# Kernel tuning notes

Hardware: AMD Instinct MI355X
Metric: run time of the kernel (lower is better)

The kernel has to match this reference:

```python
import jax, jax.numpy as jnp
import numpy as np

T = 4096          # timesteps
INPUT_DIM = 360   # n_static + 9*n_dynamic + 8
H2 = 512          # hidden2 (startMap out)
E = 128           # embed_size
H = 1024          # hidden_dim
OUT = 512         # output_dim


def setup_inputs() -> dict:
    key = jax.random.key(0)
    ks = jax.random.split(key, 9)

    def p(k, shape, fan_in):
        return (jax.random.normal(k, shape, dtype=jnp.float32) / np.float32(np.sqrt(fan_in)))

    return {
        "inputVecs": jax.random.normal(ks[0], (T, INPUT_DIM), dtype=jnp.float32),
        # startMap: Linear(input_dim -> hidden2)
        "Ws": p(ks[1], (H2, INPUT_DIM), INPUT_DIM),
        "bs": jnp.zeros((H2,), jnp.float32),
        # LSTM layer 1: input = hidden2 + embed_size
        "W_ih1": p(ks[2], (4 * H, H2 + E), H2 + E),
        "W_hh1": p(ks[3], (4 * H, H), H),
        "b_ih1": jnp.zeros((4 * H,), jnp.float32),
        "b_hh1": jnp.zeros((4 * H,), jnp.float32),
        # LSTM layer 2: input = hidden_dim
        "W_ih2": p(ks[4], (4 * H, H), H),
        "W_hh2": p(ks[5], (4 * H, H), H),
        "b_ih2": jnp.zeros((4 * H,), jnp.float32),
        "b_hh2": jnp.zeros((4 * H,), jnp.float32),
        # linear: Linear(hidden_dim -> output_dim)
        "Wl": p(ks[6], (OUT, H), H),
        "bl": jnp.zeros((OUT,), jnp.float32),
        # map: Linear(output_dim -> embed_size)
        "Wm": p(ks[7], (E, OUT), OUT),
        "bm": jnp.zeros((E,), jnp.float32),
    }


def _lstm_cell(x, h, c, W_ih, W_hh, b_ih, b_hh):
    # torch LSTM gate order: i, f, g, o
    gates = W_ih @ x + b_ih + W_hh @ h + b_hh
    i, f, g, o = jnp.split(gates, 4)
    c_new = jax.nn.sigmoid(f) * c + jax.nn.sigmoid(i) * jnp.tanh(g)
    h_new = jax.nn.sigmoid(o) * jnp.tanh(c_new)
    return h_new, c_new


def reference(inputVecs, Ws, bs, W_ih1, W_hh1, b_ih1, b_hh1,
              W_ih2, W_hh2, b_ih2, b_hh2, Wl, bl, Wm, bm):
    H_ = W_hh1.shape[1]
    E_ = Wm.shape[0]

    def step(carry, x_t):
        h1, c1, h2, c2, embed = carry
        feat = Ws @ x_t + bs                       # [H2]
        inp = jnp.concatenate([feat, embed])       # [H2+E]
        h1, c1 = _lstm_cell(inp, h1, c1, W_ih1, W_hh1, b_ih1, b_hh1)
        h2, c2 = _lstm_cell(h1, h2, c2, W_ih2, W_hh2, b_ih2, b_hh2)
        y = Wl @ h2 + bl                           # [OUT]
        new_embed = Wm @ jax.nn.log_softmax(y) + bm  # feedback embed for next step
        return (h1, c1, h2, c2, new_embed), y

    z = jnp.zeros((H_,), inputVecs.dtype)
    init = (z, z, z, z, jnp.zeros((E_,), inputVecs.dtype))
    _, ys = jax.lax.scan(step, init, inputVecs)    # ys: [T, OUT]
    return jax.nn.log_softmax(ys, axis=1)
```

## Files before the change

kernel.cpp:

```cpp
#include <hip/hip_runtime.h>
#include <math.h>


#define T_STEPS 4096
#define NWG 256

typedef unsigned u32x4 __attribute__((ext_vector_type(4)));

#define WS_RH1   0
#define WS_RH2   16384
#define WS_RY    32768
#define WS_ZERO_BYTES 40960
#define WS_FEAT  40960

#define OFF_WA 2560
#define OFF_WB 18944
#define OFF_WY 31232
#define SMEM_FLOATS 33280
#define SMEM_BYTES  (SMEM_FLOATS*4)

#define PIN4(v) asm volatile("" : "+v"((v).x), "+v"((v).y), "+v"((v).z), "+v"((v).w))
#define PIN1(v) asm volatile("" : "+v"(v))
#define FMA4(acc,s,v4) {(acc).x += (s)*(v4).x; (acc).y += (s)*(v4).y; (acc).z += (s)*(v4).z; (acc).w += (s)*(v4).w;}
#define DOT4(a,b) ((a).x*(b).x + (a).y*(b).y + (a).z*(b).z + (a).w*(b).w)

__device__ __forceinline__ u32x4 ld16(const u32x4* p){
  u32x4 r;
  asm volatile("global_load_dwordx4 %0, %1, off sc0 sc1\n\ts_waitcnt vmcnt(0)"
               : "=v"(r) : "v"(p) : "memory");
  return r;
}
__device__ __forceinline__ void ld16x4(const u32x4* p, u32x4& r0, u32x4& r1,
                                       u32x4& r2, u32x4& r3){
  asm volatile("global_load_dwordx4 %0, %4, off sc0 sc1\n\t"
               "global_load_dwordx4 %1, %4, off offset:16 sc0 sc1\n\t"
               "global_load_dwordx4 %2, %4, off offset:32 sc0 sc1\n\t"
               "global_load_dwordx4 %3, %4, off offset:48 sc0 sc1\n\t"
               "s_waitcnt vmcnt(0)"
               : "=&v"(r0), "=&v"(r1), "=&v"(r2), "=&v"(r3)
               : "v"(p) : "memory");
}
__device__ __forceinline__ void st16(u32x4* p, u32x4 v){
  asm volatile("global_store_dwordx4 %0, %1, off sc0 sc1"
               :: "v"(p), "v"(v) : "memory");
}
__device__ __forceinline__ float sigm(float x){ return 1.0f/(1.0f+expf(-x)); }

__global__ __launch_bounds__(512) void feat_kernel(
    const float* __restrict__ x, const float* __restrict__ Ws,
    const float* __restrict__ bs, float* __restrict__ feat)
{
  __shared__ float s_x[16][360];
  __shared__ float s_w[512][20];
  const int bid = blockIdx.x, tid = threadIdx.x;
  const int t0 = bid * 16;
  for (int tt = 0; tt < 16; tt++)
    if (tid < 360) s_x[tt][tid] = x[(t0+tt)*360 + tid];
  float acc[16];
  #pragma unroll
  for (int i = 0; i < 16; i++) acc[i] = 0.f;
  for (int d0 = 0; d0 < 360; d0 += 16){
    const int dn = (360 - d0 < 16) ? (360 - d0) : 16;
    __syncthreads();
    if (dn == 16){
      #pragma unroll
      for (int c4 = 0; c4 < 4; c4++)
        *(float4*)&s_w[tid][c4*4] = *(const float4*)&Ws[tid*360 + d0 + c4*4];
    } else {
      for (int c = 0; c < dn; c++) s_w[tid][c] = Ws[tid*360 + d0 + c];
    }
    __syncthreads();
    for (int c = 0; c < dn; c++){
      float wv = s_w[tid][c];
      #pragma unroll
      for (int tt = 0; tt < 16; tt++) acc[tt] += wv * s_x[tt][d0 + c];
    }
  }
  for (int tt = 0; tt < 16; tt++)
    feat[(t0+tt)*512 + tid] = acc[tt] + bs[tid];
}

__global__ __launch_bounds__(64) void ls_kernel(float* __restrict__ out)
{
  const int t = blockIdx.x, l = threadIdx.x;
  float v[8];
  #pragma unroll
  for (int i = 0; i < 8; i++) v[i] = out[t*512 + l*8 + i];
  float m0 = v[0];
  #pragma unroll
  for (int i = 1; i < 8; i++) m0 = fmaxf(m0, v[i]);
  #pragma unroll
  for (int mk = 32; mk; mk >>= 1) m0 = fmaxf(m0, __shfl_xor(m0, mk));
  float s = 0.f;
  #pragma unroll
  for (int i = 0; i < 8; i++) s += expf(v[i] - m0);
  #pragma unroll
  for (int mk = 32; mk; mk >>= 1) s += __shfl_xor(s, mk);
  float lse = m0 + logf(s);
  #pragma unroll
  for (int i = 0; i < 8; i++) out[t*512 + l*8 + i] = v[i] - lse;
}

__global__ __launch_bounds__(512, 1) void lstm_persist(
    const float* __restrict__ Wih1, const float* __restrict__ Whh1,
    const float* __restrict__ Wih2, const float* __restrict__ Whh2,
    const float* __restrict__ Wl,   const float* __restrict__ Wm,
    const float* __restrict__ bih1, const float* __restrict__ bhh1,
    const float* __restrict__ bih2, const float* __restrict__ bhh2,
    const float* __restrict__ blp,  const float* __restrict__ bmp,
    char* __restrict__ wsb, float* __restrict__ out)
{
  extern __shared__ float smem[];
  float* s_in = smem;
  float* wa   = smem + OFF_WA;
  float* wb   = smem + OFF_WB;
  float* wy   = smem + OFF_WY;
  __shared__ float s_part[16];
  __shared__ float s_sums[32];

  u32x4* rh1 = (u32x4*)(wsb + WS_RH1);
  u32x4* rh2 = (u32x4*)(wsb + WS_RH2);
  u32x4* ry  = (u32x4*)(wsb + WS_RY);
  const float* featp = (const float*)(wsb + WS_FEAT);

  const int wid = blockIdx.x, tid = threadIdx.x;
  const int w = tid >> 6, l = tid & 63;
  const int o0 = 2*w, o1 = 2*w + 1;
  const int rA0 = (o0 >> 2)*1024 + wid*4 + (o0 & 3);
  const int rA1 = (o1 >> 2)*1024 + wid*4 + (o1 & 3);

  for (int idx = tid; idx < 2048; idx += 512){
    int o = idx >> 7, e = idx & 127;
    int r = (o >> 2)*1024 + wid*4 + (o & 3);
    s_in[idx] = Wih1[r*640 + 512 + e];
  }
  __syncthreads();

  {
    float4 a00 = {0,0,0,0}, a01 = a00, a10 = a00, a11 = a00;
    for (int e = 0; e < 128; e++){
      float w0e = s_in[o0*128 + e], w1e = s_in[o1*128 + e];
      float4 m0 = *(const float4*)&Wm[e*512 + l*4];
      float4 m1 = *(const float4*)&Wm[e*512 + l*4 + 256];
      FMA4(a00, w0e, m0); FMA4(a01, w0e, m1);
      FMA4(a10, w1e, m0); FMA4(a11, w1e, m1);
    }
    *(float4*)&wb[o0*512 + l*4]       = a00;
    *(float4*)&wb[o0*512 + l*4 + 256] = a01;
    *(float4*)&wb[o1*512 + l*4]       = a10;
    *(float4*)&wb[o1*512 + l*4 + 256] = a11;
  }
  __syncthreads();

  {
    float4 c00={0,0,0,0}, c01=c00, c02=c00, c03=c00;
    float4 c10=c00, c11=c00, c12=c00, c13=c00;
    float rs0=0.f, rs1=0.f, wl0=0.f, wl1=0.f;
    for (int m = 0; m < 512; m++){
      float t0 = wb[o0*512 + m], t1 = wb[o1*512 + m];
      float blm = blp[m];
      rs0 += t0; wl0 += t0*blm; rs1 += t1; wl1 += t1*blm;
      float4 q0 = *(const float4*)&Wl[m*1024 + l*4];
      float4 q1 = *(const float4*)&Wl[m*1024 + l*4 + 256];
      float4 q2 = *(const float4*)&Wl[m*1024 + l*4 + 512];
      float4 q3 = *(const float4*)&Wl[m*1024 + l*4 + 768];
      FMA4(c00,t0,q0); FMA4(c01,t0,q1); FMA4(c02,t0,q2); FMA4(c03,t0,q3);
      FMA4(c10,t1,q0); FMA4(c11,t1,q1); FMA4(c12,t1,q2); FMA4(c13,t1,q3);
    }
    *(float4*)&wa[o0*1024 + l*4      ] = c00;
    *(float4*)&wa[o0*1024 + l*4 + 256] = c01;
    *(float4*)&wa[o0*1024 + l*4 + 512] = c02;
    *(float4*)&wa[o0*1024 + l*4 + 768] = c03;
    *(float4*)&wa[o1*1024 + l*4      ] = c10;
    *(float4*)&wa[o1*1024 + l*4 + 256] = c11;
    *(float4*)&wa[o1*1024 + l*4 + 512] = c12;
    *(float4*)&wa[o1*1024 + l*4 + 768] = c13;
    if (l == 0){
      s_sums[w*4+0] = rs0; s_sums[w*4+1] = rs1;
      s_sums[w*4+2] = wl0; s_sums[w*4+3] = wl1;
    }
  }
  __syncthreads();

  float biasAreg=0.f, biasBreg=0.f, bE2reg=0.f, rsReg=0.f;
  float bl0=0.f, bl1=0.f, c1=0.f, c2=0.f;
  if (w == 0 && l < 16){
    int r = (l >> 2)*1024 + wid*4 + (l & 3);
    biasAreg = bih1[r] + bhh1[r];
    biasBreg = bih2[r] + bhh2[r];
    rsReg = s_sums[(l>>1)*4 + (l&1)];
    float acc = s_sums[(l>>1)*4 + 2 + (l&1)];
    for (int e = 0; e < 128; e++) acc += s_in[l*128 + e] * bmp[e];
    bE2reg = acc;
  }
  if (w == 0 && l == 0){ bl0 = blp[wid*2]; bl1 = blp[wid*2 + 1]; }
  __syncthreads();

  for (int idx = tid; idx < 2048; idx += 512) s_in[512 + idx] = 0.f;
  for (int o = 0; o < 16; o++){
    int r = (o >> 2)*1024 + wid*4 + (o & 3);
    for (int c = tid; c < 768; c += 512)
      wb[o*768 + c] = Whh2[r*1024 + 256 + c];
  }
  for (int idx = tid; idx < 2048; idx += 512){
    int row = idx >> 10, c = idx & 1023;
    wy[idx] = Wl[(wid*2 + row)*1024 + c];
  }

  float4 wA0[6], wA1[6], wB0[5], wB1[5];
  #pragma unroll
  for (int j = 0; j < 6; j++){
    int c = 256*j + l*4;
    wA0[j] = (c < 512) ? *(const float4*)&Wih1[rA0*640 + c]
                       : *(const float4*)&Whh1[rA0*1024 + c - 512];
    wA1[j] = (c < 512) ? *(const float4*)&Wih1[rA1*640 + c]
                       : *(const float4*)&Whh1[rA1*1024 + c - 512];
  }
  #pragma unroll
  for (int j = 0; j < 5; j++){
    int c = 256*j + l*4;
    wB0[j] = (c < 1024) ? *(const float4*)&Wih2[rA0*1024 + c]
                        : *(const float4*)&Whh2[rA0*1024 + c - 1024];
    wB1[j] = (c < 1024) ? *(const float4*)&Wih2[rA1*1024 + c]
                        : *(const float4*)&Whh2[rA1*1024 + c - 1024];
  }
  #pragma unroll
  for (int j = 0; j < 6; j++){ PIN4(wA0[j]); PIN4(wA1[j]); }
  #pragma unroll
  for (int j = 0; j < 5; j++){ PIN4(wB0[j]); PIN4(wB1[j]); }
  PIN1(biasAreg); PIN1(biasBreg); PIN1(bE2reg); PIN1(rsReg);
  PIN1(bl0); PIN1(bl1);
  __syncthreads();

  for (int t = 0; t < T_STEPS; t++){
    const int pprev = (t + 1) & 1;
    const int pcur  = t & 1;

    if (tid < 256)
      *(float2*)&s_in[tid*2] = *(const float2*)&featp[(size_t)t*512 + tid*2];
    __syncthreads();

    float acc0 = 0.f, acc1 = 0.f;
    #pragma unroll
    for (int j = 0; j < 6; j++){
      float4 xv = *(float4*)&s_in[256*j + l*4];
      acc0 += DOT4(wA0[j], xv); acc1 += DOT4(wA1[j], xv);
    }

    if (t > 0){
      const u32x4* p2 = rh2 + pprev*512 + tid;
      u32x4 b;
      for(;;){
        b = ld16(p2);
        if (b.z >= (unsigned)t) break;
        __builtin_amdgcn_s_sleep(1);
      }
      *(float2*)&s_in[1536 + 2*tid] =
          make_float2(__uint_as_float(b.x), __uint_as_float(b.y));
    }
    __syncthreads();

    if (t > 0 && w == 0){
      float y0 = 0.f, y1 = 0.f;
      #pragma unroll
      for (int i = 0; i < 4; i++){
        float4 xv = *(float4*)&s_in[1536 + 256*i + l*4];
        float4 w0 = *(float4*)&wy[256*i + l*4];
        float4 w1 = *(float4*)&wy[1024 + 256*i + l*4];
        y0 += DOT4(w0, xv); y1 += DOT4(w1, xv);
      }
      #pragma unroll
      for (int mk = 32; mk; mk >>= 1){
        y0 += __shfl_xor(y0, mk); y1 += __shfl_xor(y1, mk);
      }
      if (l == 0){
        y0 += bl0; y1 += bl1;
        *(float2*)&out[(size_t)(t-1)*512 + wid*2] = make_float2(y0, y1);
        u32x4 rec;
        rec.x = __float_as_uint(y0); rec.y = __float_as_uint(y1);
        rec.z = (unsigned)t; rec.w = 0u;
        st16(ry + pcur*256 + wid, rec);
      }
    }
    #pragma unroll
    for (int k = 0; k < 4; k++){
      float4 xv = *(float4*)&s_in[1536 + 256*k + l*4];
      float4 u0 = *(float4*)&wa[o0*1024 + 256*k + l*4];
      float4 u1 = *(float4*)&wa[o1*1024 + 256*k + l*4];
      acc0 += DOT4(u0, xv); acc1 += DOT4(u1, xv);
    }
    #pragma unroll
    for (int mk = 32; mk; mk >>= 1){
      acc0 += __shfl_xor(acc0, mk); acc1 += __shfl_xor(acc1, mk);
    }
    if (l == 0){ s_part[o0] = acc0; s_part[o1] = acc1; }

    float pB0, pB1;
    {
      float4 xv = *(float4*)&s_in[1536 + l*4];
      pB0 = DOT4(wB0[4], xv); pB1 = DOT4(wB1[4], xv);
      #pragma unroll
      for (int k = 0; k < 3; k++){
        float4 x2 = *(float4*)&s_in[1536 + 256 + 256*k + l*4];
        float4 u0 = *(float4*)&wb[o0*768 + 256*k + l*4];
        float4 u1 = *(float4*)&wb[o1*768 + 256*k + l*4];
        pB0 += DOT4(u0, x2); pB1 += DOT4(u1, x2);
      }
    }
    __syncthreads();

    if (w == 0){
      float lse = 0.f;
      if (t > 0){
        const u32x4* pyr = ry + pcur*256 + 4*l;
        u32x4 r0, r1, r2, r3;
        for(;;){
          ld16x4(pyr, r0, r1, r2, r3);
          if (r0.z >= (unsigned)t && r1.z >= (unsigned)t &&
              r2.z >= (unsigned)t && r3.z >= (unsigned)t) break;
          __builtin_amdgcn_s_sleep(1);
        }
        float v0 = __uint_as_float(r0.x), v1 = __uint_as_float(r0.y);
        float v2 = __uint_as_float(r1.x), v3 = __uint_as_float(r1.y);
        float v4 = __uint_as_float(r2.x), v5 = __uint_as_float(r2.y);
        float v6 = __uint_as_float(r3.x), v7 = __uint_as_float(r3.y);
        float m0 = fmaxf(fmaxf(fmaxf(v0,v1), fmaxf(v2,v3)),
                         fmaxf(fmaxf(v4,v5), fmaxf(v6,v7)));
        #pragma unroll
        for (int mk = 32; mk; mk >>= 1) m0 = fmaxf(m0, __shfl_xor(m0, mk));
        float s = expf(v0-m0)+expf(v1-m0)+expf(v2-m0)+expf(v3-m0)
                + expf(v4-m0)+expf(v5-m0)+expf(v6-m0)+expf(v7-m0);
        #pragma unroll
        for (int mk = 32; mk; mk >>= 1) s += __shfl_xor(s, mk);
        lse = m0 + logf(s);
      }
      float hn = 0.f;
      if (l < 16){
        float sum = s_part[l] + biasAreg;
        if (t > 0) sum += bE2reg - rsReg*lse;
        float gi = __shfl(sum, (l & 3));
        float gf = __shfl(sum, 4 + (l & 3));
        float gg = __shfl(sum, 8 + (l & 3));
        float go = __shfl(sum, 12 + (l & 3));
        if (l < 4){
          float cn = sigm(gf)*c1 + sigm(gi)*tanhf(gg);
          c1 = cn;
          hn = sigm(go)*tanhf(cn);
        }
      }
      float g0 = __shfl(hn, 2*(l & 1));
      float g1 = __shfl(hn, 2*(l & 1) + 1);
      if (l < 2){
        u32x4 rec;
        rec.x = __float_as_uint(g0); rec.y = __float_as_uint(g1);
        rec.z = (unsigned)(t + 1); rec.w = 0u;
        st16(rh1 + pcur*512 + wid*2 + l, rec);
      }
    }

    {
      const u32x4* p1 = rh1 + pcur*512 + tid;
      u32x4 a;
      for(;;){
        a = ld16(p1);
        if (a.z >= (unsigned)(t + 1)) break;
        __builtin_amdgcn_s_sleep(1);
      }
      *(float2*)&s_in[512 + 2*tid] =
          make_float2(__uint_as_float(a.x), __uint_as_float(a.y));
    }
    __syncthreads();

    float b0 = pB0, b1 = pB1;
    #pragma unroll
    for (int j = 0; j < 4; j++){
      float4 xv = *(float4*)&s_in[512 + 256*j + l*4];
      b0 += DOT4(wB0[j], xv); b1 += DOT4(wB1[j], xv);
    }
    #pragma unroll
    for (int mk = 32; mk; mk >>= 1){
      b0 += __shfl_xor(b0, mk); b1 += __shfl_xor(b1, mk);
    }
    if (l == 0){ s_part[o0] = b0; s_part[o1] = b1; }
    __syncthreads();

    if (w == 0){
      float hn = 0.f;
      if (l < 16){
        float sum = s_part[l] + biasBreg;
        float gi = __shfl(sum, (l & 3));
        float gf = __shfl(sum, 4 + (l & 3));
        float gg = __shfl(sum, 8 + (l & 3));
        float go = __shfl(sum, 12 + (l & 3));
        if (l < 4){
          float cn = sigm(gf)*c2 + sigm(gi)*tanhf(gg);
          c2 = cn;
          hn = sigm(go)*tanhf(cn);
        }
      }
      float g0 = __shfl(hn, 2*(l & 1));
      float g1 = __shfl(hn, 2*(l & 1) + 1);
      if (l < 2){
        u32x4 rec;
        rec.x = __float_as_uint(g0); rec.y = __float_as_uint(g1);
        rec.z = (unsigned)(t + 1); rec.w = 0u;
        st16(rh2 + pcur*512 + wid*2 + l, rec);
      }
    }
  }

  {
    const u32x4* p2 = rh2 + ((T_STEPS - 1) & 1)*512 + tid;
    u32x4 b;
    for(;;){
      b = ld16(p2);
      if (b.z >= (unsigned)T_STEPS) break;
      __builtin_amdgcn_s_sleep(1);
    }
    *(float2*)&s_in[1536 + 2*tid] =
        make_float2(__uint_as_float(b.x), __uint_as_float(b.y));
  }
  __syncthreads();
  if (w == 0){
    float y0 = 0.f, y1 = 0.f;
    #pragma unroll
    for (int i = 0; i < 4; i++){
      float4 xv = *(float4*)&s_in[1536 + 256*i + l*4];
      float4 w0 = *(float4*)&wy[256*i + l*4];
      float4 w1 = *(float4*)&wy[1024 + 256*i + l*4];
      y0 += DOT4(w0, xv); y1 += DOT4(w1, xv);
    }
    #pragma unroll
    for (int mk = 32; mk; mk >>= 1){
      y0 += __shfl_xor(y0, mk); y1 += __shfl_xor(y1, mk);
    }
    if (l == 0)
      *(float2*)&out[(size_t)(T_STEPS-1)*512 + wid*2] =
          make_float2(y0 + bl0, y1 + bl1);
  }
}

extern "C" void kernel_launch(void* const* d_in, const int* in_sizes, int n_in,
                              void* d_out, int out_size, void* d_ws, size_t ws_size,
                              hipStream_t stream)
{
  const float* x    = (const float*)d_in[0];
  const float* Ws   = (const float*)d_in[1];
  const float* bs   = (const float*)d_in[2];
  const float* Wih1 = (const float*)d_in[3];
  const float* Whh1 = (const float*)d_in[4];
  const float* bih1 = (const float*)d_in[5];
  const float* bhh1 = (const float*)d_in[6];
  const float* Wih2 = (const float*)d_in[7];
  const float* Whh2 = (const float*)d_in[8];
  const float* bih2 = (const float*)d_in[9];
  const float* bhh2 = (const float*)d_in[10];
  const float* Wl   = (const float*)d_in[11];
  const float* bl   = (const float*)d_in[12];
  const float* Wm   = (const float*)d_in[13];
  const float* bm   = (const float*)d_in[14];
  char* wsb  = (char*)d_ws;
  float* out = (float*)d_out;

  hipMemsetAsync(wsb, 0, WS_ZERO_BYTES, stream);

  feat_kernel<<<256, 512, 0, stream>>>(x, Ws, bs, (float*)(wsb + WS_FEAT));
  lstm_persist<<<NWG, 512, SMEM_BYTES, stream>>>(
      Wih1, Whh1, Wih2, Whh2, Wl, Wm,
      bih1, bhh1, bih2, bhh2, bl, bm, wsb, out);
  ls_kernel<<<T_STEPS, 64, 0, stream>>>(out);
}
```

Baseline: 25.11 ms.

## Publish layer-1 pre-activations before lse and apply lse correction redundantly per block

Each workgroup now publishes its raw layer-1 gate pre-activations (without the log-softmax correction) plus its previous cell state to global memory, instead of waiting for the lse reduction before computing and publishing h1. Every workgroup then gathers all gates, applies the per-gate lse correction using precomputed vectors derived from W_ih1 embed columns and Wm column sums, and evaluates the LSTM nonlinearity for all 1024 units redundantly. This takes the lse wait off the critical path of the cross-workgroup handoff, so it overlaps with the exchange. In exchange it doubles the exchanged bytes per step, adds redundant transcendental work in every block, and adds a long setup pass computing the correction vectors.

New measurement: 66.04 ms. 2.63x slower.

```diff
diff --git a/kernel.cpp b/kernel.cpp
--- a/kernel.cpp
+++ b/kernel.cpp
@@ -7,11 +7,11 @@
 
 typedef unsigned u32x4 __attribute__((ext_vector_type(4)));
 
-#define WS_RH1   0
-#define WS_RH2   16384
-#define WS_RY    32768
-#define WS_ZERO_BYTES 40960
-#define WS_FEAT  40960
+#define WS_RG1   0
+#define WS_RH2   65536
+#define WS_RY    81920
+#define WS_ZERO_BYTES 90112
+#define WS_FEAT  90112
 
 #define OFF_WA 2560
 #define OFF_WB 18944
@@ -117,8 +117,11 @@
   float* wy   = smem + OFF_WY;
   __shared__ float s_part[16];
   __shared__ float s_sums[32];
-
-  u32x4* rh1 = (u32x4*)(wsb + WS_RH1);
+  __shared__ float s_cs[128];
+  __shared__ float s_lse[1];
+  __shared__ float s_c1[4];
+
+  u32x4* rg1 = (u32x4*)(wsb + WS_RG1);
   u32x4* rh2 = (u32x4*)(wsb + WS_RH2);
   u32x4* ry  = (u32x4*)(wsb + WS_RY);
   const float* featp = (const float*)(wsb + WS_FEAT);
@@ -133,6 +136,14 @@
     int o = idx >> 7, e = idx & 127;
     int r = (o >> 2)*1024 + wid*4 + (o & 3);
     s_in[idx] = Wih1[r*640 + 512 + e];
+  }
+  if (tid < 128){
+    float s = 0.f;
+    for (int m = 0; m < 512; m += 4){
+      float4 v = *(const float4*)&Wm[tid*512 + m];
+      s += v.x + v.y + v.z + v.w;
+    }
+    s_cs[tid] = s;
   }
   __syncthreads();
 
@@ -155,11 +166,11 @@
   {
     float4 c00={0,0,0,0}, c01=c00, c02=c00, c03=c00;
     float4 c10=c00, c11=c00, c12=c00, c13=c00;
-    float rs0=0.f, rs1=0.f, wl0=0.f, wl1=0.f;
+    float wl0=0.f, wl1=0.f;
     for (int m = 0; m < 512; m++){
       float t0 = wb[o0*512 + m], t1 = wb[o1*512 + m];
       float blm = blp[m];
-      rs0 += t0; wl0 += t0*blm; rs1 += t1; wl1 += t1*blm;
+      wl0 += t0*blm; wl1 += t1*blm;
       float4 q0 = *(const float4*)&Wl[m*1024 + l*4];
       float4 q1 = *(const float4*)&Wl[m*1024 + l*4 + 256];
       float4 q2 = *(const float4*)&Wl[m*1024 + l*4 + 512];
@@ -175,25 +186,43 @@
     *(float4*)&wa[o1*1024 + l*4 + 256] = c11;
     *(float4*)&wa[o1*1024 + l*4 + 512] = c12;
     *(float4*)&wa[o1*1024 + l*4 + 768] = c13;
-    if (l == 0){
-      s_sums[w*4+0] = rs0; s_sums[w*4+1] = rs1;
-      s_sums[w*4+2] = wl0; s_sums[w*4+3] = wl1;
-    }
+    if (l == 0){ s_sums[w*2+0] = wl0; s_sums[w*2+1] = wl1; }
   }
   __syncthreads();
 
-  float biasAreg=0.f, biasBreg=0.f, bE2reg=0.f, rsReg=0.f;
-  float bl0=0.f, bl1=0.f, c1=0.f, c2=0.f;
+  float biasAreg=0.f, biasBreg=0.f, bE2reg=0.f;
+  float bl0=0.f, bl1=0.f, c2=0.f;
   if (w == 0 && l < 16){
     int r = (l >> 2)*1024 + wid*4 + (l & 3);
     biasAreg = bih1[r] + bhh1[r];
     biasBreg = bih2[r] + bhh2[r];
-    rsReg = s_sums[(l>>1)*4 + (l&1)];
-    float acc = s_sums[(l>>1)*4 + 2 + (l&1)];
+    float acc = s_sums[(l>>1)*2 + (l&1)];
     for (int e = 0; e < 128; e++) acc += s_in[l*128 + e] * bmp[e];
     bE2reg = acc;
   }
   if (w == 0 && l == 0){ bl0 = blp[wid*2]; bl1 = blp[wid*2 + 1]; }
+  if (w == 0 && l < 4) s_c1[l] = 0.f;
+  float4 dE0, dE1;
+  {
+    float dv[8];
+    #pragma unroll
+    for (int j = 0; j < 2; j++){
+      int e = 2*tid + j;
+      #pragma unroll
+      for (int k = 0; k < 4; k++){
+        int r = k*1024 + e;
+        float s = 0.f;
+        for (int ee = 0; ee < 128; ee += 4){
+          float4 wv = *(const float4*)&Wih1[(size_t)r*640 + 512 + ee];
+          float4 cv = *(const float4*)&s_cs[ee];
+          s += DOT4(wv, cv);
+        }
+        dv[j*4 + k] = s;
+      }
+    }
+    dE0 = make_float4(dv[0], dv[1], dv[2], dv[3]);
+    dE1 = make_float4(dv[4], dv[5], dv[6], dv[7]);
+  }
   __syncthreads();
 
   for (int idx = tid; idx < 2048; idx += 512) s_in[512 + idx] = 0.f;
@@ -228,13 +257,15 @@
   for (int j = 0; j < 6; j++){ PIN4(wA0[j]); PIN4(wA1[j]); }
   #pragma unroll
   for (int j = 0; j < 5; j++){ PIN4(wB0[j]); PIN4(wB1[j]); }
-  PIN1(biasAreg); PIN1(biasBreg); PIN1(bE2reg); PIN1(rsReg);
+  PIN4(dE0); PIN4(dE1);
+  PIN1(biasAreg); PIN1(biasBreg); PIN1(bE2reg);
   PIN1(bl0); PIN1(bl1);
   __syncthreads();
 
   for (int t = 0; t < T_STEPS; t++){
     const int pprev = (t + 1) & 1;
     const int pcur  = t & 1;
+    const unsigned need = (unsigned)(t + 1);
 
     if (tid < 256)
       *(float2*)&s_in[tid*2] = *(const float2*)&featp[(size_t)t*512 + tid*2];
@@ -309,65 +340,82 @@
     }
     __syncthreads();
 
-    if (w == 0){
-      float lse = 0.f;
+    if (w == 0 && l < 16){
+      float sum = s_part[l] + biasAreg;
+      if (t > 0) sum += bE2reg;
+      float gi = __shfl(sum, (l & 3));
+      float gf = __shfl(sum, 4 + (l & 3));
+      float gg = __shfl(sum, 8 + (l & 3));
+      float go = __shfl(sum, 12 + (l & 3));
+      if (l < 4){
+        u32x4 rA, rB;
+        rA.x = __float_as_uint(gi); rA.y = __float_as_uint(gf);
+        rA.z = __float_as_uint(gg); rA.w = need;
+        rB.x = __float_as_uint(go); rB.y = __float_as_uint(s_c1[l]);
+        rB.z = need; rB.w = 0u;
+        int base = pcur*2048 + (wid*4 + l)*2;
+        st16(rg1 + base,     rA);
+        st16(rg1 + base + 1, rB);
+      }
+    }
+
+    if (w == 0 && t > 0){
+      const u32x4* pyr = ry + pcur*256 + 4*l;
+      u32x4 q0, q1, q2, q3;
+      for(;;){
+        ld16x4(pyr, q0, q1, q2, q3);
+        if (q0.z >= (unsigned)t && q1.z >= (unsigned)t &&
+            q2.z >= (unsigned)t && q3.z >= (unsigned)t) break;
+        __builtin_amdgcn_s_sleep(1);
+      }
+      float v0 = __uint_as_float(q0.x), v1 = __uint_as_float(q0.y);
+      float v2 = __uint_as_float(q1.x), v3 = __uint_as_float(q1.y);
+      float v4 = __uint_as_float(q2.x), v5 = __uint_as_float(q2.y);
+      float v6 = __uint_as_float(q3.x), v7 = __uint_as_float(q3.y);
+      float m0 = fmaxf(fmaxf(fmaxf(v0,v1), fmaxf(v2,v3)),
+                       fmaxf(fmaxf(v4,v5), fmaxf(v6,v7)));
+      #pragma unroll
+      for (int mk = 32; mk; mk >>= 1) m0 = fmaxf(m0, __shfl_xor(m0, mk));
+      float s = expf(v0-m0)+expf(v1-m0)+expf(v2-m0)+expf(v3-m0)
+              + expf(v4-m0)+expf(v5-m0)+expf(v6-m0)+expf(v7-m0);
+      #pragma unroll
+      for (int mk = 32; mk; mk >>= 1) s += __shfl_xor(s, mk);
+      if (l == 0) s_lse[0] = m0 + logf(s);
+    }
+    u32x4 r0, r1, r2, r3;
+    {
+      const u32x4* pg = rg1 + pcur*2048 + 4*tid;
+      for(;;){
+        ld16x4(pg, r0, r1, r2, r3);
+        if (r0.w >= need && r1.z >= need &&
+            r2.w >= need && r3.z >= need) break;
+        __builtin_amdgcn_s_sleep(1);
+      }
+    }
+    __syncthreads();
+
+    {
+      float lse = s_lse[0];
+      float i0 = __uint_as_float(r0.x), f0 = __uint_as_float(r0.y);
+      float g0 = __uint_as_float(r0.z);
+      float oo0 = __uint_as_float(r1.x), cp0 = __uint_as_float(r1.y);
+      float i1 = __uint_as_float(r2.x), f1 = __uint_as_float(r2.y);
+      float g1 = __uint_as_float(r2.z);
+      float oo1 = __uint_as_float(r3.x), cp1 = __uint_as_float(r3.y);
       if (t > 0){
-        const u32x4* pyr = ry + pcur*256 + 4*l;
-        u32x4 r0, r1, r2, r3;
-        for(;;){
-          ld16x4(pyr, r0, r1, r2, r3);
-          if (r0.z >= (unsigned)t && r1.z >= (unsigned)t &&
-              r2.z >= (unsigned)t && r3.z >= (unsigned)t) break;
-          __builtin_amdgcn_s_sleep(1);
-        }
-        float v0 = __uint_as_float(r0.x), v1 = __uint_as_float(r0.y);
-        float v2 = __uint_as_float(r1.x), v3 = __uint_as_float(r1.y);
-        float v4 = __uint_as_float(r2.x), v5 = __uint_as_float(r2.y);
-        float v6 = __uint_as_float(r3.x), v7 = __uint_as_float(r3.y);
-        float m0 = fmaxf(fmaxf(fmaxf(v0,v1), fmaxf(v2,v3)),
-                         fmaxf(fmaxf(v4,v5), fmaxf(v6,v7)));
-        #pragma unroll
-        for (int mk = 32; mk; mk >>= 1) m0 = fmaxf(m0, __shfl_xor(m0, mk));
-        float s = expf(v0-m0)+expf(v1-m0)+expf(v2-m0)+expf(v3-m0)
-                + expf(v4-m0)+expf(v5-m0)+expf(v6-m0)+expf(v7-m0);
-        #pragma unroll
-        for (int mk = 32; mk; mk >>= 1) s += __shfl_xor(s, mk);
-        lse = m0 + logf(s);
-      }
-      float hn = 0.f;
-      if (l < 16){
-        float sum = s_part[l] + biasAreg;
-        if (t > 0) sum += bE2reg - rsReg*lse;
-        float gi = __shfl(sum, (l & 3));
-        float gf = __shfl(sum, 4 + (l & 3));
-        float gg = __shfl(sum, 8 + (l & 3));
-        float go = __shfl(sum, 12 + (l & 3));
-        if (l < 4){
-          float cn = sigm(gf)*c1 + sigm(gi)*tanhf(gg);
-          c1 = cn;
-          hn = sigm(go)*tanhf(cn);
-        }
-      }
-      float g0 = __shfl(hn, 2*(l & 1));
-      float g1 = __shfl(hn, 2*(l & 1) + 1);
-      if (l < 2){
-        u32x4 rec;
-        rec.x = __float_as_uint(g0); rec.y = __float_as_uint(g1);
-        rec.z = (unsigned)(t + 1); rec.w = 0u;
-        st16(rh1 + pcur*512 + wid*2 + l, rec);
-      }
-    }
-
-    {
-      const u32x4* p1 = rh1 + pcur*512 + tid;
-      u32x4 a;
-      for(;;){
-        a = ld16(p1);
-        if (a.z >= (unsigned)(t + 1)) break;
-        __builtin_amdgcn_s_sleep(1);
-      }
-      *(float2*)&s_in[512 + 2*tid] =
-          make_float2(__uint_as_float(a.x), __uint_as_float(a.y));
+        i0 -= dE0.x*lse; f0 -= dE0.y*lse; g0 -= dE0.z*lse; oo0 -= dE0.w*lse;
+        i1 -= dE1.x*lse; f1 -= dE1.y*lse; g1 -= dE1.z*lse; oo1 -= dE1.w*lse;
+      }
+      float cn0 = sigm(f0)*cp0 + sigm(i0)*tanhf(g0);
+      float h0  = sigm(oo0)*tanhf(cn0);
+      float cn1 = sigm(f1)*cp1 + sigm(i1)*tanhf(g1);
+      float h1v = sigm(oo1)*tanhf(cn1);
+      s_in[512 + 2*tid]     = h0;
+      s_in[512 + 2*tid + 1] = h1v;
+      if ((tid >> 1) == wid){
+        s_c1[2*(tid & 1)]     = cn0;
+        s_c1[2*(tid & 1) + 1] = cn1;
+      }
     }
     __syncthreads();
 
@@ -403,7 +451,7 @@
       if (l < 2){
         u32x4 rec;
         rec.x = __float_as_uint(g0); rec.y = __float_as_uint(g1);
-        rec.z = (unsigned)(t + 1); rec.w = 0u;
+        rec.z = need; rec.w = 0u;
         st16(rh2 + pcur*512 + wid*2 + l, rec);
       }
     }
```

## Pipeline spin-wait polls and prefetch next-step features into the recurrence loop

Applied to the files above, without the earlier changes.

Replaces the sleep-based one-load-at-a-time spin loops with a poll that keeps two global loads in flight, and drops s_sleep from the y poll loop, cutting wake-up latency on cross-workgroup flags. The next timestep's feature vector is now loaded while waiting on the h1 flag and written to shared memory before an existing barrier, which removes one __syncthreads per step. The row-sum precomputation also moves out of the main setup loop. The cost is more memory traffic from polling and possibly more contention on the flag lines.

After: 31.30 ms. 1.25x slower.

```diff
diff --git a/kernel.cpp b/kernel.cpp
--- a/kernel.cpp
+++ b/kernel.cpp
@@ -24,12 +24,6 @@
 #define FMA4(acc,s,v4) {(acc).x += (s)*(v4).x; (acc).y += (s)*(v4).y; (acc).z += (s)*(v4).z; (acc).w += (s)*(v4).w;}
 #define DOT4(a,b) ((a).x*(b).x + (a).y*(b).y + (a).z*(b).z + (a).w*(b).w)
 
-__device__ __forceinline__ u32x4 ld16(const u32x4* p){
-  u32x4 r;
-  asm volatile("global_load_dwordx4 %0, %1, off sc0 sc1\n\ts_waitcnt vmcnt(0)"
-               : "=v"(r) : "v"(p) : "memory");
-  return r;
-}
 __device__ __forceinline__ void ld16x4(const u32x4* p, u32x4& r0, u32x4& r1,
                                        u32x4& r2, u32x4& r3){
   asm volatile("global_load_dwordx4 %0, %4, off sc0 sc1\n\t"
@@ -43,6 +37,20 @@
 __device__ __forceinline__ void st16(u32x4* p, u32x4 v){
   asm volatile("global_store_dwordx4 %0, %1, off sc0 sc1"
                :: "v"(p), "v"(v) : "memory");
+}
+__device__ __forceinline__ u32x4 pollrec(const u32x4* p, unsigned need){
+  u32x4 a, b;
+  asm volatile("global_load_dwordx4 %0, %1, off sc0 sc1" : "=v"(a) : "v"(p));
+  for(;;){
+    asm volatile("global_load_dwordx4 %0, %1, off sc0 sc1" : "=v"(b) : "v"(p));
+    asm volatile("s_waitcnt vmcnt(1)" : "+v"(a) :: "memory");
+    if (a.z >= need) break;
+    asm volatile("global_load_dwordx4 %0, %1, off sc0 sc1" : "=v"(a) : "v"(p));
+    asm volatile("s_waitcnt vmcnt(1)" : "+v"(b) :: "memory");
+    if (b.z >= need){ a = b; break; }
+  }
+  asm volatile("s_waitcnt vmcnt(0)" ::: "memory");
+  return a;
 }
 __device__ __forceinline__ float sigm(float x){ return 1.0f/(1.0f+expf(-x)); }
 
@@ -155,11 +163,11 @@
   {
     float4 c00={0,0,0,0}, c01=c00, c02=c00, c03=c00;
     float4 c10=c00, c11=c00, c12=c00, c13=c00;
-    float rs0=0.f, rs1=0.f, wl0=0.f, wl1=0.f;
+    float wl0=0.f, wl1=0.f;
     for (int m = 0; m < 512; m++){
       float t0 = wb[o0*512 + m], t1 = wb[o1*512 + m];
       float blm = blp[m];
-      rs0 += t0; wl0 += t0*blm; rs1 += t1; wl1 += t1*blm;
+      wl0 += t0*blm; wl1 += t1*blm;
       float4 q0 = *(const float4*)&Wl[m*1024 + l*4];
       float4 q1 = *(const float4*)&Wl[m*1024 + l*4 + 256];
       float4 q2 = *(const float4*)&Wl[m*1024 + l*4 + 512];
@@ -175,10 +183,7 @@
     *(float4*)&wa[o1*1024 + l*4 + 256] = c11;
     *(float4*)&wa[o1*1024 + l*4 + 512] = c12;
     *(float4*)&wa[o1*1024 + l*4 + 768] = c13;
-    if (l == 0){
-      s_sums[w*4+0] = rs0; s_sums[w*4+1] = rs1;
-      s_sums[w*4+2] = wl0; s_sums[w*4+3] = wl1;
-    }
+    if (l == 0){ s_sums[w*2+0] = wl0; s_sums[w*2+1] = wl1; }
   }
   __syncthreads();
 
@@ -188,15 +193,22 @@
     int r = (l >> 2)*1024 + wid*4 + (l & 3);
     biasAreg = bih1[r] + bhh1[r];
     biasBreg = bih2[r] + bhh2[r];
-    rsReg = s_sums[(l>>1)*4 + (l&1)];
-    float acc = s_sums[(l>>1)*4 + 2 + (l&1)];
+    float acc = s_sums[(l>>1)*2 + (l&1)];
     for (int e = 0; e < 128; e++) acc += s_in[l*128 + e] * bmp[e];
     bE2reg = acc;
+    float rsum = 0.f;
+    for (int m = 0; m < 512; m += 4){
+      float4 v = *(float4*)&wb[l*512 + m];
+      rsum += v.x + v.y + v.z + v.w;
+    }
+    rsReg = rsum;
   }
   if (w == 0 && l == 0){ bl0 = blp[wid*2]; bl1 = blp[wid*2 + 1]; }
   __syncthreads();
 
   for (int idx = tid; idx < 2048; idx += 512) s_in[512 + idx] = 0.f;
+  if (tid < 256)
+    *(float2*)&s_in[tid*2] = *(const float2*)&featp[tid*2];
   for (int o = 0; o < 16; o++){
     int r = (o >> 2)*1024 + wid*4 + (o & 3);
     for (int c = tid; c < 768; c += 512)
@@ -236,10 +248,6 @@
     const int pprev = (t + 1) & 1;
     const int pcur  = t & 1;
 
-    if (tid < 256)
-      *(float2*)&s_in[tid*2] = *(const float2*)&featp[(size_t)t*512 + tid*2];
-    __syncthreads();
-
     float acc0 = 0.f, acc1 = 0.f;
     #pragma unroll
     for (int j = 0; j < 6; j++){
@@ -248,13 +256,7 @@
     }
 
     if (t > 0){
-      const u32x4* p2 = rh2 + pprev*512 + tid;
-      u32x4 b;
-      for(;;){
-        b = ld16(p2);
-        if (b.z >= (unsigned)t) break;
-        __builtin_amdgcn_s_sleep(1);
-      }
+      u32x4 b = pollrec(rh2 + pprev*512 + tid, (unsigned)t);
       *(float2*)&s_in[1536 + 2*tid] =
           make_float2(__uint_as_float(b.x), __uint_as_float(b.y));
     }
@@ -318,7 +320,6 @@
           ld16x4(pyr, r0, r1, r2, r3);
           if (r0.z >= (unsigned)t && r1.z >= (unsigned)t &&
               r2.z >= (unsigned)t && r3.z >= (unsigned)t) break;
-          __builtin_amdgcn_s_sleep(1);
         }
         float v0 = __uint_as_float(r0.x), v1 = __uint_as_float(r0.y);
         float v2 = __uint_as_float(r1.x), v3 = __uint_as_float(r1.y);
@@ -358,17 +359,17 @@
       }
     }
 
+    float2 fv;
+    if (tid < 256){
+      int tn = (t + 1 < T_STEPS) ? (t + 1) : t;
+      fv = *(const float2*)&featp[(size_t)tn*512 + tid*2];
+    }
     {
-      const u32x4* p1 = rh1 + pcur*512 + tid;
-      u32x4 a;
-      for(;;){
-        a = ld16(p1);
-        if (a.z >= (unsigned)(t + 1)) break;
-        __builtin_amdgcn_s_sleep(1);
-      }
+      u32x4 a = pollrec(rh1 + pcur*512 + tid, (unsigned)(t + 1));
       *(float2*)&s_in[512 + 2*tid] =
           make_float2(__uint_as_float(a.x), __uint_as_float(a.y));
     }
+    if (tid < 256) *(float2*)&s_in[tid*2] = fv;
     __syncthreads();
 
     float b0 = pB0, b1 = pB1;
@@ -410,13 +411,7 @@
   }
 
   {
-    const u32x4* p2 = rh2 + ((T_STEPS - 1) & 1)*512 + tid;
-    u32x4 b;
-    for(;;){
-      b = ld16(p2);
-      if (b.z >= (unsigned)T_STEPS) break;
-      __builtin_amdgcn_s_sleep(1);
-    }
+    u32x4 b = pollrec(rh2 + ((T_STEPS - 1) & 1)*512 + tid, (unsigned)T_STEPS);
     *(float2*)&s_in[1536 + 2*tid] =
         make_float2(__uint_as_float(b.x), __uint_as_float(b.y));
   }
```
